# Optimization experiments

Hardware: AMD Instinct MI355X
Metric: run time of the kernel (lower is better)

Reference implementation:

```python
import jax, jax.numpy as jnp
import numpy as np

BN_EPS = 1e-5
OUT_H, OUT_W = 32, 32  # crop_size / output_stride = 512/16


def setup_inputs() -> dict:
    key = jax.random.key(0)
    k1, k2, k3, k4 = jax.random.split(key, 4)
    x = jax.random.normal(k1, (16, 2048, 32, 32), dtype=jnp.float32)
    # conv1x1 weight, bias-free: [dim_out, dim_in]
    W = jax.random.normal(k2, (256, 2048), dtype=jnp.float32) * (1.0 / np.sqrt(2048.0))
    gamma = jax.random.normal(k3, (256,), dtype=jnp.float32) * 0.1 + 1.0
    beta = jax.random.normal(k4, (256,), dtype=jnp.float32) * 0.1
    return {"x": x, "W": W, "gamma": gamma, "beta": beta}


def reference(x, W, gamma, beta):
    # 1x1 conv, no bias: channel contraction
    y = jnp.einsum("nchw,oc->nohw", x, W)  # [N, dim_out, H, W]
    # BatchNorm2d in training mode: batch statistics over (N, H, W), biased var
    mean = jnp.mean(y, axis=(0, 2, 3), keepdims=True)
    var = jnp.mean(jnp.square(y - mean), axis=(0, 2, 3), keepdims=True)
    g = gamma.reshape(1, -1, 1, 1)
    b = beta.reshape(1, -1, 1, 1)
    y = g * (y - mean) * jax.lax.rsqrt(var + BN_EPS) + b
    # global average pool to 1x1
    pooled = jnp.mean(y, axis=(2, 3), keepdims=True)  # [N, dim_out, 1, 1]
    # adaptive avg pool from 1x1 to (OUT_H, OUT_W) is a pure broadcast
    out = jnp.broadcast_to(pooled, pooled.shape[:2] + (OUT_H, OUT_W))
    return out
```

## Files before the change

kernel.cpp:

```cpp
#include <hip/hip_runtime.h>
#include <hip/hip_bf16.h>
#include <stdint.h>

#define NB   16
#define CIN  2048
#define OUTC 256
#define HW   1024
#define BJ   64
#define BK   64
#define NJT  (HW / BJ)
#define KSTEPS (CIN / BK)

typedef __attribute__((ext_vector_type(8))) short bf16x8;
typedef __attribute__((ext_vector_type(4))) float f32x4;
typedef __attribute__((ext_vector_type(4))) unsigned int u32x4;

__device__ __forceinline__ unsigned int f2bf(float f) {
    union { float f; unsigned int u; } a; a.f = f;
    return (a.u + 0x7FFFu + ((a.u >> 16) & 1u)) >> 16;
}

__device__ __forceinline__ void block_sync_lds() {
    asm volatile("s_waitcnt lgkmcnt(0)" ::: "memory");
    __builtin_amdgcn_s_barrier();
    asm volatile("" ::: "memory");
}

__global__ void wprep_kernel(const float* __restrict__ W, unsigned short* __restrict__ Afrag) {
    int g  = blockIdx.x * blockDim.x + threadIdx.x;
    int o  = g >> 8;
    int kc = g & 255;
    const float4* p = reinterpret_cast<const float4*>(W + o * CIN + kc * 8);
    float4 v0 = p[0], v1 = p[1];
    u32x4 pk;
    pk.x = f2bf(v0.x) | (f2bf(v0.y) << 16);
    pk.y = f2bf(v0.z) | (f2bf(v0.w) << 16);
    pk.z = f2bf(v1.x) | (f2bf(v1.y) << 16);
    pk.w = f2bf(v1.z) | (f2bf(v1.w) << 16);
    int ks32 = kc >> 2, g8 = kc & 3;
    int lane = g8 * 16 + (o & 15), ot = o >> 4;
    *reinterpret_cast<u32x4*>(Afrag + (((size_t)ks32 * 16 + ot) * 64 + lane) * 8) = pk;
}

__global__ __launch_bounds__(512, 2) void gemm_stats_kernel(
    const float* __restrict__ x,
    const unsigned short* __restrict__ Afrag,
    float* __restrict__ s1_part,
    float* __restrict__ s2_part)
{
    __shared__ __align__(16) unsigned short B0[4096], B1[4096];

    const int tid  = threadIdx.x;
    const int lane = tid & 63;
    const int wave = tid >> 6;
    const int blk  = blockIdx.x;
    const int n    = blk >> 4;
    const int jt   = blk & 15;
    const int j0   = jt * BJ;

    const float* xn = x + (size_t)n * CIN * HW;

    const int bj = tid & 63;
    const int kh = tid >> 6;
    const float* Bgp = xn + (size_t)(kh * 8) * HW + j0 + bj;
    const int offB = (kh >> 2) * 2048 + (bj >> 4) * 512 + (bj & 15) * 32
                   + ((kh & 3) ^ (bj & 3)) * 8;

    const int rA = lane & 15;
    const int gX = (lane >> 4) ^ (rA & 3);
    const int roffB = rA * 32 + gX * 8;

    const unsigned short* Ab = Afrag + (size_t)lane * 8;

#define LDA(ks, R) { _Pragma("unroll") \
    for (int h = 0; h < 2; ++h) _Pragma("unroll") for (int t = 0; t < 2; ++t) \
        R[h * 2 + t] = *(const u32x4*)(Ab + ((((ks) * 2 + h) * 16 + 2 * wave + t) * 64) * 8); }
#define LDB(ks, F) { const float* p = Bgp + (size_t)(ks) * BK * HW; \
    _Pragma("unroll") for (int i = 0; i < 8; ++i) F[i] = p[(size_t)i * HW]; }
#define WRITEB(Bb, F) { u32x4 pk; \
    pk.x = f2bf(F[0]) | (f2bf(F[1]) << 16); pk.y = f2bf(F[2]) | (f2bf(F[3]) << 16); \
    pk.z = f2bf(F[4]) | (f2bf(F[5]) << 16); pk.w = f2bf(F[6]) | (f2bf(F[7]) << 16); \
    *(u32x4*)&Bb[offB] = pk; }
#define COMPUTE(Bb, R) { _Pragma("unroll") \
    for (int h = 0; h < 2; ++h) { \
        bf16x8 af0 = *(const bf16x8*)&R[h * 2 + 0]; \
        bf16x8 af1 = *(const bf16x8*)&R[h * 2 + 1]; \
        _Pragma("unroll") \
        for (int ni = 0; ni < 4; ++ni) { \
            bf16x8 bf = *(const bf16x8*)&Bb[h * 2048 + ni * 512 + roffB]; \
            acc[0][ni] = __builtin_amdgcn_mfma_f32_16x16x32_bf16(af0, bf, acc[0][ni], 0, 0, 0); \
            acc[1][ni] = __builtin_amdgcn_mfma_f32_16x16x32_bf16(af1, bf, acc[1][ni], 0, 0, 0); \
    } } }

    f32x4 acc[2][4] = {};
    u32x4 Aa0[4], Aa1[4];
    float Bs0[8], Bs1[8];

    LDA(0, Aa0); LDB(0, Bs0);
    LDA(1, Aa1); LDB(1, Bs1);
    WRITEB(B0, Bs0);
    LDB(2, Bs0);
    block_sync_lds();

    #pragma unroll 1
    for (int ks = 0; ks < KSTEPS; ks += 2) {
        COMPUTE(B0, Aa0);
        {
            int ka = (ks + 2 < KSTEPS) ? ks + 2 : KSTEPS - 1;
            LDA(ka, Aa0);
            WRITEB(B1, Bs1);
            int kb = (ks + 3 < KSTEPS) ? ks + 3 : KSTEPS - 1;
            LDB(kb, Bs1);
            block_sync_lds();
        }
        COMPUTE(B1, Aa1);
        if (ks + 2 < KSTEPS) {
            int ka = (ks + 3 < KSTEPS) ? ks + 3 : KSTEPS - 1;
            LDA(ka, Aa1);
            WRITEB(B0, Bs0);
            int kb = (ks + 4 < KSTEPS) ? ks + 4 : KSTEPS - 1;
            LDB(kb, Bs0);
            block_sync_lds();
        }
    }

    float rs[2][4], rq[2][4];
    #pragma unroll
    for (int mi = 0; mi < 2; ++mi) {
        #pragma unroll
        for (int r = 0; r < 4; ++r) {
            float s = 0.f, q = 0.f;
            #pragma unroll
            for (int ni = 0; ni < 4; ++ni) {
                float v = acc[mi][ni][r];
                s += v; q += v * v;
            }
            rs[mi][r] = s; rq[mi][r] = q;
        }
    }
    #pragma unroll
    for (int m = 1; m < 16; m <<= 1) {
        #pragma unroll
        for (int mi = 0; mi < 2; ++mi) {
            #pragma unroll
            for (int r = 0; r < 4; ++r) {
                rs[mi][r] += __shfl_xor(rs[mi][r], m, 64);
                rq[mi][r] += __shfl_xor(rq[mi][r], m, 64);
            }
        }
    }
    if (rA == 0) {
        const int gK = lane >> 4;
        #pragma unroll
        for (int mi = 0; mi < 2; ++mi) {
            #pragma unroll
            for (int r = 0; r < 4; ++r) {
                int o = wave * 32 + mi * 16 + gK * 4 + r;
                s1_part[(jt * NB + n) * OUTC + o] = rs[mi][r];
                s2_part[blk * OUTC + o]           = rq[mi][r];
            }
        }
    }
#undef LDA
#undef LDB
#undef WRITEB
#undef COMPUTE
}

__global__ __launch_bounds__(256) void finalize_bcast_kernel(
    const float* __restrict__ s1_part,
    const float* __restrict__ s2_part,
    const float* __restrict__ gamma,
    const float* __restrict__ beta,
    float* __restrict__ out)
{
    const int tid   = threadIdx.x;
    const int slice = tid & 15;
    const int o_l   = tid >> 4;
    const int n0    = blockIdx.x >> 4;
    const int o     = (blockIdx.x & 15) * 16 + o_l;

    float S1 = 0.f, S2 = 0.f;
    #pragma unroll
    for (int q = 0; q < 16; ++q) {
        int p = slice * 16 + q;
        S1 += s1_part[p * OUTC + o];
        S2 += s2_part[p * OUTC + o];
    }
    float s1n = s1_part[(slice * NB + n0) * OUTC + o];
    #pragma unroll
    for (int m = 1; m < 16; m <<= 1) {
        S1  += __shfl_xor(S1, m, 64);
        S2  += __shfl_xor(S2, m, 64);
        s1n += __shfl_xor(s1n, m, 64);
    }
    float mean = S1 * (1.f / 16384.f);
    float var  = S2 * (1.f / 16384.f) - mean * mean;
    float inv  = rsqrtf(var + 1e-5f);
    float v = gamma[o] * (s1n * (1.f / 1024.f) - mean) * inv + beta[o];

    float4 vv = make_float4(v, v, v, v);
    float4* dst = reinterpret_cast<float4*>(out + ((size_t)(n0 * OUTC + o)) * HW);
    #pragma unroll
    for (int it = 0; it < 16; ++it)
        dst[it * 16 + slice] = vv;
}

extern "C" void kernel_launch(void* const* d_in, const int* in_sizes, int n_in,
                              void* d_out, int out_size, void* d_ws, size_t ws_size,
                              hipStream_t stream) {
    const float* x     = (const float*)d_in[0];
    const float* W     = (const float*)d_in[1];
    const float* gamma = (const float*)d_in[2];
    const float* beta  = (const float*)d_in[3];
    float* out = (float*)d_out;

    char* ws = (char*)d_ws;
    unsigned short* Afrag = (unsigned short*)ws;
    float* s1_part = (float*)(ws + (1 << 20));
    float* s2_part = (float*)(ws + (1 << 20) + (256 << 10));

    hipLaunchKernelGGL(wprep_kernel, dim3(256), dim3(256), 0, stream, W, Afrag);
    hipLaunchKernelGGL(gemm_stats_kernel, dim3(256), dim3(512), 0, stream,
                       x, Afrag, s1_part, s2_part);
    hipLaunchKernelGGL(finalize_bcast_kernel, dim3(NB * (OUTC / 16)), dim3(256), 0, stream,
                       s1_part, s2_part, gamma, beta, out);
}
```

Measured before the change: 49.15 us.

## Halve spatial tile to 32 and use 4-wave blocks with 64 channels each

Shrinks the GEMM block's spatial tile from 64 to 32 columns and drops the block to 256 threads, so there are 512 blocks instead of 256. Each wave now covers 64 output channels with a 4x2 MFMA accumulator grid and a single A register set that is reloaded each half-step. The aim is more blocks to fill the CUs and less LDS per block. The finalize kernel now sums 32 partials per slice, and the s2 workspace offset moves. The cost is that each A fragment is reused across fewer spatial columns, so more A traffic from L2 per FLOP, and the A prefetch is no longer double buffered.

After: 55.61 us. 13.1% more time.

```diff
diff --git a/kernel.cpp b/kernel.cpp
--- a/kernel.cpp
+++ b/kernel.cpp
@@ -6,7 +6,7 @@
 #define CIN  2048
 #define OUTC 256
 #define HW   1024
-#define BJ   64
+#define BJ   32
 #define BK   64
 #define NJT  (HW / BJ)
 #define KSTEPS (CIN / BK)
@@ -42,28 +42,28 @@
     *reinterpret_cast<u32x4*>(Afrag + (((size_t)ks32 * 16 + ot) * 64 + lane) * 8) = pk;
 }
 
-__global__ __launch_bounds__(512, 2) void gemm_stats_kernel(
+__global__ __launch_bounds__(256, 2) void gemm_stats_kernel(
     const float* __restrict__ x,
     const unsigned short* __restrict__ Afrag,
     float* __restrict__ s1_part,
     float* __restrict__ s2_part)
 {
-    __shared__ __align__(16) unsigned short B0[4096], B1[4096];
+    __shared__ __align__(16) unsigned short B0[2048], B1[2048];
 
     const int tid  = threadIdx.x;
     const int lane = tid & 63;
     const int wave = tid >> 6;
     const int blk  = blockIdx.x;
-    const int n    = blk >> 4;
-    const int jt   = blk & 15;
+    const int n    = blk >> 5;
+    const int jt   = blk & 31;
     const int j0   = jt * BJ;
 
     const float* xn = x + (size_t)n * CIN * HW;
 
-    const int bj = tid & 63;
-    const int kh = tid >> 6;
+    const int bj = tid & 31;
+    const int kh = tid >> 5;
     const float* Bgp = xn + (size_t)(kh * 8) * HW + j0 + bj;
-    const int offB = (kh >> 2) * 2048 + (bj >> 4) * 512 + (bj & 15) * 32
+    const int offB = (kh >> 2) * 1024 + (bj >> 4) * 512 + (bj & 15) * 32
                    + ((kh & 3) ^ (bj & 3)) * 8;
 
     const int rA = lane & 15;
@@ -73,8 +73,8 @@
     const unsigned short* Ab = Afrag + (size_t)lane * 8;
 
 #define LDA(ks, R) { _Pragma("unroll") \
-    for (int h = 0; h < 2; ++h) _Pragma("unroll") for (int t = 0; t < 2; ++t) \
-        R[h * 2 + t] = *(const u32x4*)(Ab + ((((ks) * 2 + h) * 16 + 2 * wave + t) * 64) * 8); }
+    for (int h = 0; h < 2; ++h) _Pragma("unroll") for (int mi = 0; mi < 4; ++mi) \
+        R[h * 4 + mi] = *(const u32x4*)(Ab + ((((ks) * 2 + h) * 16 + wave * 4 + mi) * 64) * 8); }
 #define LDB(ks, F) { const float* p = Bgp + (size_t)(ks) * BK * HW; \
     _Pragma("unroll") for (int i = 0; i < 8; ++i) F[i] = p[(size_t)i * HW]; }
 #define WRITEB(Bb, F) { u32x4 pk; \
@@ -82,41 +82,40 @@
     pk.z = f2bf(F[4]) | (f2bf(F[5]) << 16); pk.w = f2bf(F[6]) | (f2bf(F[7]) << 16); \
     *(u32x4*)&Bb[offB] = pk; }
 #define COMPUTE(Bb, R) { _Pragma("unroll") \
-    for (int h = 0; h < 2; ++h) { \
-        bf16x8 af0 = *(const bf16x8*)&R[h * 2 + 0]; \
-        bf16x8 af1 = *(const bf16x8*)&R[h * 2 + 1]; \
+    for (int h = 0; h < 2; ++h) _Pragma("unroll") for (int ni = 0; ni < 2; ++ni) { \
+        bf16x8 bf = *(const bf16x8*)&Bb[h * 1024 + ni * 512 + roffB]; \
         _Pragma("unroll") \
-        for (int ni = 0; ni < 4; ++ni) { \
-            bf16x8 bf = *(const bf16x8*)&Bb[h * 2048 + ni * 512 + roffB]; \
-            acc[0][ni] = __builtin_amdgcn_mfma_f32_16x16x32_bf16(af0, bf, acc[0][ni], 0, 0, 0); \
-            acc[1][ni] = __builtin_amdgcn_mfma_f32_16x16x32_bf16(af1, bf, acc[1][ni], 0, 0, 0); \
+        for (int mi = 0; mi < 4; ++mi) { \
+            bf16x8 af = *(const bf16x8*)&R[h * 4 + mi]; \
+            acc[mi][ni] = __builtin_amdgcn_mfma_f32_16x16x32_bf16(af, bf, acc[mi][ni], 0, 0, 0); \
     } } }
 
-    f32x4 acc[2][4] = {};
-    u32x4 Aa0[4], Aa1[4];
+    f32x4 acc[4][2] = {};
+    u32x4 Ra[8];
     float Bs0[8], Bs1[8];
 
-    LDA(0, Aa0); LDB(0, Bs0);
-    LDA(1, Aa1); LDB(1, Bs1);
+    LDA(0, Ra);
+    LDB(0, Bs0); LDB(1, Bs1);
     WRITEB(B0, Bs0);
     LDB(2, Bs0);
     block_sync_lds();
 
     #pragma unroll 1
     for (int ks = 0; ks < KSTEPS; ks += 2) {
-        COMPUTE(B0, Aa0);
+        COMPUTE(B0, Ra);
+        LDA(ks + 1, Ra);
+        WRITEB(B1, Bs1);
+        {
+            int kb = (ks + 3 < KSTEPS) ? ks + 3 : KSTEPS - 1;
+            LDB(kb, Bs1);
+        }
+        block_sync_lds();
+        COMPUTE(B1, Ra);
         {
             int ka = (ks + 2 < KSTEPS) ? ks + 2 : KSTEPS - 1;
-            LDA(ka, Aa0);
-            WRITEB(B1, Bs1);
-            int kb = (ks + 3 < KSTEPS) ? ks + 3 : KSTEPS - 1;
-            LDB(kb, Bs1);
-            block_sync_lds();
-        }
-        COMPUTE(B1, Aa1);
+            LDA(ka, Ra);
+        }
         if (ks + 2 < KSTEPS) {
-            int ka = (ks + 3 < KSTEPS) ? ks + 3 : KSTEPS - 1;
-            LDA(ka, Aa1);
             WRITEB(B0, Bs0);
             int kb = (ks + 4 < KSTEPS) ? ks + 4 : KSTEPS - 1;
             LDB(kb, Bs0);
@@ -124,24 +123,20 @@
         }
     }
 
-    float rs[2][4], rq[2][4];
-    #pragma unroll
-    for (int mi = 0; mi < 2; ++mi) {
+    float rs[4][4], rq[4][4];
+    #pragma unroll
+    for (int mi = 0; mi < 4; ++mi) {
         #pragma unroll
         for (int r = 0; r < 4; ++r) {
-            float s = 0.f, q = 0.f;
-            #pragma unroll
-            for (int ni = 0; ni < 4; ++ni) {
-                float v = acc[mi][ni][r];
-                s += v; q += v * v;
-            }
-            rs[mi][r] = s; rq[mi][r] = q;
+            float v0 = acc[mi][0][r], v1 = acc[mi][1][r];
+            rs[mi][r] = v0 + v1;
+            rq[mi][r] = v0 * v0 + v1 * v1;
         }
     }
     #pragma unroll
     for (int m = 1; m < 16; m <<= 1) {
         #pragma unroll
-        for (int mi = 0; mi < 2; ++mi) {
+        for (int mi = 0; mi < 4; ++mi) {
             #pragma unroll
             for (int r = 0; r < 4; ++r) {
                 rs[mi][r] += __shfl_xor(rs[mi][r], m, 64);
@@ -152,10 +147,10 @@
     if (rA == 0) {
         const int gK = lane >> 4;
         #pragma unroll
-        for (int mi = 0; mi < 2; ++mi) {
+        for (int mi = 0; mi < 4; ++mi) {
             #pragma unroll
             for (int r = 0; r < 4; ++r) {
-                int o = wave * 32 + mi * 16 + gK * 4 + r;
+                int o = wave * 64 + mi * 16 + gK * 4 + r;
                 s1_part[(jt * NB + n) * OUTC + o] = rs[mi][r];
                 s2_part[blk * OUTC + o]           = rq[mi][r];
             }
@@ -182,12 +177,13 @@
 
     float S1 = 0.f, S2 = 0.f;
     #pragma unroll
-    for (int q = 0; q < 16; ++q) {
-        int p = slice * 16 + q;
+    for (int q = 0; q < 32; ++q) {
+        int p = slice * 32 + q;
         S1 += s1_part[p * OUTC + o];
         S2 += s2_part[p * OUTC + o];
     }
-    float s1n = s1_part[(slice * NB + n0) * OUTC + o];
+    float s1n = s1_part[(slice * 2 * NB + n0) * OUTC + o]
+              + s1_part[((slice * 2 + 1) * NB + n0) * OUTC + o];
     #pragma unroll
     for (int m = 1; m < 16; m <<= 1) {
         S1  += __shfl_xor(S1, m, 64);
@@ -218,10 +214,10 @@
     char* ws = (char*)d_ws;
     unsigned short* Afrag = (unsigned short*)ws;
     float* s1_part = (float*)(ws + (1 << 20));
-    float* s2_part = (float*)(ws + (1 << 20) + (256 << 10));
+    float* s2_part = (float*)(ws + (1 << 20) + (512 << 10));
 
     hipLaunchKernelGGL(wprep_kernel, dim3(256), dim3(256), 0, stream, W, Afrag);
-    hipLaunchKernelGGL(gemm_stats_kernel, dim3(256), dim3(512), 0, stream,
+    hipLaunchKernelGGL(gemm_stats_kernel, dim3(NB * NJT), dim3(256), 0, stream,
                        x, Afrag, s1_part, s2_part);
     hipLaunchKernelGGL(finalize_bcast_kernel, dim3(NB * (OUTC / 16)), dim3(256), 0, stream,
                        s1_part, s2_part, gamma, beta, out);
```
